# Performance work log

Hardware: AMD Instinct MI355X
Metric: run time of the kernel (lower is better)

The kernel has to match this reference:

```python
import jax, jax.numpy as jnp
import numpy as np

D_MODEL = 1024
NUM_HEADS = 16
D_K = D_MODEL // NUM_HEADS
ROPE_THETA = 10000.0
SEQ = 4096


def setup_inputs() -> dict:
    key = jax.random.key(0)
    ks = jax.random.split(key, 5)
    s = 1.0 / np.sqrt(D_MODEL)
    return {
        "x": jax.random.normal(ks[0], (1, SEQ, D_MODEL), jnp.float32),
        "token_positions": jnp.arange(SEQ, dtype=jnp.int32),
        "Wq": jax.random.normal(ks[1], (D_MODEL, D_MODEL), jnp.float32) * s,
        "Wk": jax.random.normal(ks[2], (D_MODEL, D_MODEL), jnp.float32) * s,
        "Wv": jax.random.normal(ks[3], (D_MODEL, D_MODEL), jnp.float32) * s,
        "Wo": jax.random.normal(ks[4], (D_MODEL, D_MODEL), jnp.float32) * s,
    }


def _rope(t, positions):
    # t: [b, h, s, d_k]; interleaved pair rotation
    half = D_K // 2
    inv_freq = ROPE_THETA ** (-jnp.arange(half, dtype=jnp.float32) * 2.0 / D_K)
    ang = positions.astype(jnp.float32)[:, None] * inv_freq[None, :]  # [s, half]
    cos, sin = jnp.cos(ang), jnp.sin(ang)
    x1 = t[..., 0::2]
    x2 = t[..., 1::2]
    r1 = x1 * cos - x2 * sin
    r2 = x1 * sin + x2 * cos
    return jnp.stack([r1, r2], axis=-1).reshape(t.shape)


def reference(x, token_positions, Wq, Wk, Wv, Wo):
    b, s, _ = x.shape
    def split_heads(t):
        return t.reshape(b, s, NUM_HEADS, D_K).transpose(0, 2, 1, 3)  # [b,h,s,dk]
    q = split_heads(x @ Wq.T)
    k = split_heads(x @ Wk.T)
    v = split_heads(x @ Wv.T)
    q = _rope(q, token_positions)
    k = _rope(k, token_positions)
    scores = jnp.einsum('bhqd,bhkd->bhqk', q, k) / np.sqrt(D_K)
    causal = jnp.tril(jnp.ones((s, s), dtype=bool))
    scores = jnp.where(causal, scores, -jnp.inf)
    attn = jax.nn.softmax(scores, axis=-1)
    out = jnp.einsum('bhqk,bhkd->bhqd', attn, v)
    out = out.transpose(0, 2, 1, 3).reshape(b, s, D_MODEL)
    return out @ Wo.T
```

## Files before the change

kernel.cpp:

```cpp
#include <hip/hip_runtime.h>

#define S    4096
#define DM   1024
#define H    16
#define DK   64

typedef __bf16 bf16;
typedef __bf16 bf16x8 __attribute__((ext_vector_type(8)));
typedef __bf16 bf16x4 __attribute__((ext_vector_type(4)));
typedef float  f32x4  __attribute__((ext_vector_type(4)));

__global__ __launch_bounds__(256)
void convert_kernel(const float* __restrict__ x,  const float* __restrict__ wq,
                    const float* __restrict__ wk, const float* __restrict__ wv,
                    const float* __restrict__ wo,
                    bf16* __restrict__ xb,  bf16* __restrict__ wqb,
                    bf16* __restrict__ wkb, bf16* __restrict__ wvb,
                    bf16* __restrict__ wob)
{
    const size_t i = (size_t)blockIdx.x * 256 + threadIdx.x;
    const float* src; bf16* dst; size_t off;
    if (i < 1048576)      { src = x;  dst = xb;  off = i; }
    else if (i < 1310720) { src = wq; dst = wqb; off = i - 1048576; }
    else if (i < 1572864) { src = wk; dst = wkb; off = i - 1310720; }
    else if (i < 1835008) { src = wv; dst = wvb; off = i - 1572864; }
    else                  { src = wo; dst = wob; off = i - 1835008; }
    f32x4 v = ((const f32x4*)src)[off];
    bf16x4 b;
    for (int r = 0; r < 4; r++) b[r] = (bf16)v[r];
    ((bf16x4*)dst)[off] = b;
}

__global__ __launch_bounds__(256)
void gemm_kernel(const bf16* __restrict__ A,
                 const bf16* __restrict__ w0, const bf16* __restrict__ w1,
                 const bf16* __restrict__ w2,
                 const int* __restrict__ pos,
                 bf16* __restrict__ o0, bf16* __restrict__ o1,
                 bf16* __restrict__ o2,
                 float* __restrict__ of,
                 int base_mode)
{
    const int z    = blockIdx.z;
    const int mode = base_mode + z;
    const bf16* W  = (z == 0) ? w0 : (z == 1 ? w1 : w2);
    bf16* Out      = (z == 0) ? o0 : (z == 1 ? o1 : o2);

    __shared__ bf16 As[64 * 72];
    __shared__ bf16 Bs[64 * 72];

    const int tid  = threadIdx.x;
    const int lane = tid & 63;
    const int wv   = tid >> 6;
    const int quad = lane >> 4;
    const int col  = lane & 15;
    const int wm   = wv >> 1, wn = wv & 1;

    const int tileM = blockIdx.x * 64;
    const int tileN = blockIdx.y * 64;

    const int ldRow = tid >> 2;
    const int ldK   = (tid & 3) * 16;

    f32x4 acc[2][2] = {};

    for (int kc = 0; kc < DM; kc += 64) {
        bf16x8 a0 = *(const bf16x8*)&A[(size_t)(tileM + ldRow) * DM + kc + ldK];
        bf16x8 a1 = *(const bf16x8*)&A[(size_t)(tileM + ldRow) * DM + kc + ldK + 8];
        bf16x8 b0 = *(const bf16x8*)&W[(size_t)(tileN + ldRow) * DM + kc + ldK];
        bf16x8 b1 = *(const bf16x8*)&W[(size_t)(tileN + ldRow) * DM + kc + ldK + 8];
        __syncthreads();
        *(bf16x8*)&As[ldRow * 72 + ldK]     = a0;
        *(bf16x8*)&As[ldRow * 72 + ldK + 8] = a1;
        *(bf16x8*)&Bs[ldRow * 72 + ldK]     = b0;
        *(bf16x8*)&Bs[ldRow * 72 + ldK + 8] = b1;
        __syncthreads();

        for (int kk = 0; kk < 2; kk++) {
            bf16x8 af0 = *(const bf16x8*)&As[(wm * 32 + 0 * 16 + col) * 72 + kk * 32 + quad * 8];
            bf16x8 af1 = *(const bf16x8*)&As[(wm * 32 + 1 * 16 + col) * 72 + kk * 32 + quad * 8];
            bf16x8 bf0 = *(const bf16x8*)&Bs[(wn * 32 + 0 * 16 + col) * 72 + kk * 32 + quad * 8];
            bf16x8 bf1 = *(const bf16x8*)&Bs[(wn * 32 + 1 * 16 + col) * 72 + kk * 32 + quad * 8];

            acc[0][0] = __builtin_amdgcn_mfma_f32_16x16x32_bf16(af0, bf0, acc[0][0], 0, 0, 0);
            acc[0][1] = __builtin_amdgcn_mfma_f32_16x16x32_bf16(af0, bf1, acc[0][1], 0, 0, 0);
            acc[1][0] = __builtin_amdgcn_mfma_f32_16x16x32_bf16(af1, bf0, acc[1][0], 0, 0, 0);
            acc[1][1] = __builtin_amdgcn_mfma_f32_16x16x32_bf16(af1, bf1, acc[1][1], 0, 0, 0);
        }
    }

    for (int fm = 0; fm < 2; fm++)
    for (int fn = 0; fn < 2; fn++) {
        f32x4 v = acc[fm][fn];
        const int n = tileN + wn * 32 + fn * 16 + col;
        for (int r = 0; r < 4; r++) {
            const int m = tileM + wm * 32 + fm * 16 + quad * 4 + r;
            float val = v[r];
            if (mode <= 1) {
                float part = __shfl_xor(val, 1);
                const int d = n & 63;
                const int i = d >> 1;
                float inv = exp2f(-(float)i * 0.41524101186092034f);
                float ang = (float)pos[m] * inv;
                float c = cosf(ang), sn = sinf(ang);
                float rot = (n & 1) ? (val * c + part * sn)
                                    : (val * c - part * sn);
                if (mode == 0) rot *= 0.18033688011112042f;
                Out[((size_t)(n >> 6) * S + m) * 64 + d] = (bf16)rot;
            } else if (mode == 2) {
                Out[(size_t)n * S + m] = (bf16)val;
            } else {
                of[(size_t)m * DM + n] = val;
            }
        }
    }
}

__global__ __launch_bounds__(256, 2)
void attn_kernel(const bf16* __restrict__ q, const bf16* __restrict__ k,
                 const bf16* __restrict__ vt,
                 bf16* __restrict__ P0g, bf16* __restrict__ P1g,
                 float* __restrict__ l0g, float* __restrict__ l1g)
{
    const int bid = blockIdx.x;
    const int xcd = bid & 7;
    const int b3  = (bid >> 3) & 1;
    const int u   = (bid >> 4) & 15;
    const int b8  = (bid >> 8) & 1;
    const int h   = (xcd << 1) | b8;
    const int z   = b3;
    const int QB  = (b3 == b8) ? (15 - u) : u;

    const int tid  = threadIdx.x;
    const int lane = tid & 63;
    const int wv   = tid >> 6;
    const int quad = lane >> 4;
    const int col  = lane & 15;

    const int T2  = 2 * QB + 2;
    const int kt0 = z * T2;
    const int kt1 = kt0 + T2;

    __shared__ bf16 Ks[64 * 72];
    __shared__ bf16 Vs[64 * 72];
    __shared__ bf16 plds[4][64 * 40];

    const int qbase = QB * 256 + wv * 64;

    bf16x8 qf[4][2];
#pragma unroll
    for (int qt = 0; qt < 4; qt++) {
        const bf16* qr = &q[((size_t)(h * S + qbase + qt * 16 + col)) * 64];
        qf[qt][0] = *(const bf16x8*)(qr + quad * 8);
        qf[qt][1] = *(const bf16x8*)(qr + 32 + quad * 8);
    }

    float li[4] = {};
    f32x4 o[4][4] = {};

    const int srow = tid >> 2;
    const int sseg = (tid & 3) * 16;
    const bf16* kg_ = k  + ((size_t)h * S) * 64;
    const bf16* vg_ = vt + ((size_t)h * 64) * S;

    bf16x8 kr0 = *(const bf16x8*)(kg_ + (size_t)(kt0 * 64 + srow) * 64 + sseg);
    bf16x8 kr1 = *(const bf16x8*)(kg_ + (size_t)(kt0 * 64 + srow) * 64 + sseg + 8);
    bf16x8 vr0 = *(const bf16x8*)(vg_ + (size_t)srow * S + kt0 * 64 + sseg);
    bf16x8 vr1 = *(const bf16x8*)(vg_ + (size_t)srow * S + kt0 * 64 + sseg + 8);

    for (int kt = kt0; kt < kt1; kt++) {
        const int kbase = kt * 64;

        __syncthreads();
        *(bf16x8*)&Ks[srow * 72 + sseg]     = kr0;
        *(bf16x8*)&Ks[srow * 72 + sseg + 8] = kr1;
        *(bf16x8*)&Vs[srow * 72 + sseg]     = vr0;
        *(bf16x8*)&Vs[srow * 72 + sseg + 8] = vr1;
        __syncthreads();

        if (kt + 1 < kt1) {
            const int nb = kbase + 64;
            kr0 = *(const bf16x8*)(kg_ + (size_t)(nb + srow) * 64 + sseg);
            kr1 = *(const bf16x8*)(kg_ + (size_t)(nb + srow) * 64 + sseg + 8);
            vr0 = *(const bf16x8*)(vg_ + (size_t)srow * S + nb + sseg);
            vr1 = *(const bf16x8*)(vg_ + (size_t)srow * S + nb + sseg + 8);
        }

        const bool diag = (kt >= (QB << 2));

#pragma unroll
        for (int half = 0; half < 2; half++) {
            __builtin_amdgcn_wave_barrier();
#pragma unroll
            for (int kg2 = 0; kg2 < 2; kg2++) {
                const int kg = half * 2 + kg2;
                bf16x8 kf0 = *(const bf16x8*)&Ks[(kg * 16 + col) * 72 + quad * 8];
                bf16x8 kf1 = *(const bf16x8*)&Ks[(kg * 16 + col) * 72 + 32 + quad * 8];

                f32x4 st[4];
                __builtin_amdgcn_s_setprio(1);
#pragma unroll
                for (int qt = 0; qt < 4; qt++) {
                    f32x4 zz = {};
                    zz = __builtin_amdgcn_mfma_f32_16x16x32_bf16(kf0, qf[qt][0], zz, 0, 0, 0);
                    zz = __builtin_amdgcn_mfma_f32_16x16x32_bf16(kf1, qf[qt][1], zz, 0, 0, 0);
                    st[qt] = zz;
                }
                __builtin_amdgcn_s_setprio(0);

                if (diag) {
#pragma unroll
                    for (int qt = 0; qt < 4; qt++) {
                        const int gq = qbase + qt * 16 + col;
#pragma unroll
                        for (int r = 0; r < 4; r++) {
                            const int gk = kbase + kg * 16 + quad * 4 + r;
                            st[qt][r] = (gk > gq) ? -1e30f : st[qt][r];
                        }
                    }
                }

#pragma unroll
                for (int qt = 0; qt < 4; qt++) {
                    bf16x4 pk;
#pragma unroll
                    for (int r = 0; r < 4; r++) {
                        float p;
                        asm("v_exp_f32 %0, %1" : "=v"(p) : "v"(st[qt][r]));
                        li[qt] += p;
                        pk[r] = (bf16)p;
                    }
                    *(bf16x4*)&plds[wv][(qt * 16 + col) * 40 + kg2 * 16 + quad * 4] = pk;
                }
            }

            __builtin_amdgcn_wave_barrier();

            bf16x8 pb[4];
#pragma unroll
            for (int qt = 0; qt < 4; qt++)
                pb[qt] = *(const bf16x8*)&plds[wv][(qt * 16 + col) * 40 + quad * 8];

            __builtin_amdgcn_s_setprio(1);
#pragma unroll
            for (int dg = 0; dg < 4; dg++) {
                bf16x8 va = *(const bf16x8*)&Vs[(dg * 16 + col) * 72 + half * 32 + quad * 8];
#pragma unroll
                for (int qt = 0; qt < 4; qt++)
                    o[dg][qt] = __builtin_amdgcn_mfma_f32_16x16x32_bf16(va, pb[qt], o[dg][qt], 0, 0, 0);
            }
            __builtin_amdgcn_s_setprio(0);
        }
    }

#pragma unroll
    for (int qt = 0; qt < 4; qt++) {
        li[qt] += __shfl_xor(li[qt], 16);
        li[qt] += __shfl_xor(li[qt], 32);
    }

    bf16*  Pz = z ? P1g : P0g;
    float* lz = z ? l1g : l0g;
#pragma unroll
    for (int dg = 0; dg < 4; dg++)
#pragma unroll
    for (int qt = 0; qt < 4; qt++) {
        const int gq = qbase + qt * 16 + col;
        bf16x4 ov;
#pragma unroll
        for (int r = 0; r < 4; r++) ov[r] = (bf16)o[dg][qt][r];
        *(bf16x4*)&Pz[(size_t)gq * DM + h * 64 + dg * 16 + quad * 4] = ov;
    }
    if (quad == 0) {
#pragma unroll
        for (int qt = 0; qt < 4; qt++)
            lz[(size_t)h * S + qbase + qt * 16 + col] = li[qt];
    }
}

__global__ __launch_bounds__(256)
void combine_kernel(const bf16* __restrict__ P0, const bf16* __restrict__ P1,
                    const float* __restrict__ l0, const float* __restrict__ l1,
                    bf16* __restrict__ ao)
{
    const size_t i    = (size_t)blockIdx.x * 256 + threadIdx.x;
    const size_t base = i * 8;
    const int s  = (int)(base >> 10);
    const int dm = (int)(base & 1023);
    const int h  = dm >> 6;
    const float rli = 1.f / (l0[(size_t)h * S + s] + l1[(size_t)h * S + s]);
    bf16x8 a = *(const bf16x8*)&P0[base];
    bf16x8 b = *(const bf16x8*)&P1[base];
    bf16x8 ov;
    for (int r = 0; r < 8; r++)
        ov[r] = (bf16)(((float)a[r] + (float)b[r]) * rli);
    *(bf16x8*)&ao[base] = ov;
}

extern "C" void kernel_launch(void* const* d_in, const int* in_sizes, int n_in,
                              void* d_out, int out_size, void* d_ws, size_t ws_size,
                              hipStream_t stream)
{
    const float* x   = (const float*)d_in[0];
    const int*   pos = (const int*)d_in[1];
    const float* Wq  = (const float*)d_in[2];
    const float* Wk  = (const float*)d_in[3];
    const float* Wv  = (const float*)d_in[4];
    const float* Wo  = (const float*)d_in[5];
    float* out = (float*)d_out;

    char* w = (char*)d_ws;
    bf16*  xb  = (bf16*)(w);
    bf16*  wqb = (bf16*)(w + (size_t) 8 * 1024 * 1024);
    bf16*  wkb = (bf16*)(w + (size_t)10 * 1024 * 1024);
    bf16*  wvb = (bf16*)(w + (size_t)12 * 1024 * 1024);
    bf16*  P0  = (bf16*)(w);
    bf16*  P1  = (bf16*)(w + (size_t) 8 * 1024 * 1024);
    bf16*  qb  = (bf16*)(w + (size_t)16 * 1024 * 1024);
    bf16*  kb  = (bf16*)(w + (size_t)24 * 1024 * 1024);
    bf16*  vt  = (bf16*)(w + (size_t)32 * 1024 * 1024);
    float* l0  = (float*)(w + (size_t)40 * 1024 * 1024);
    float* l1  = (float*)(w + (size_t)40 * 1024 * 1024 + 256 * 1024);
    bf16*  ao  = (bf16*)(w + (size_t)16 * 1024 * 1024);
    bf16*  wob = (bf16*)(w + (size_t)46 * 1024 * 1024);

    dim3 blk(256);
    convert_kernel<<<dim3(8192), blk, 0, stream>>>(x, Wq, Wk, Wv, Wo,
                                                   xb, wqb, wkb, wvb, wob);
    gemm_kernel<<<dim3(64, 16, 3), blk, 0, stream>>>(xb, wqb, wkb, wvb, pos,
                                                     qb, kb, vt, out, 0);
    attn_kernel<<<dim3(512), blk, 0, stream>>>(qb, kb, vt,
                                               P0, P1, l0, l1);
    combine_kernel<<<dim3(2048), blk, 0, stream>>>(P0, P1, l0, l1, ao);
    gemm_kernel<<<dim3(64, 16, 1), blk, 0, stream>>>(ao, wob, wob, wob, pos,
                                                     P0, P0, P0, out, 3);
}
```

Before: 230.0 us.

## Enlarge GEMM tiles to 128x128 and load tiles directly to LDS

The projection GEMM tile grows from 64x64 to 128x128, so each wave computes a 4x4 grid of MFMA fragments instead of 2x2. Operand tiles are now fetched with global_load_lds straight into LDS in a fragment-ordered layout, which removes the register staging and the padded row layout. The aim is more data reuse per LDS load and fewer global loads per FLOP. In exchange the grid has fewer blocks (768 for QKV, 256 for the output projection) and each thread holds more accumulator registers.

```diff
diff --git a/kernel.cpp b/kernel.cpp
--- a/kernel.cpp
+++ b/kernel.cpp
@@ -46,8 +46,8 @@
     const bf16* W  = (z == 0) ? w0 : (z == 1 ? w1 : w2);
     bf16* Out      = (z == 0) ? o0 : (z == 1 ? o1 : o2);
 
-    __shared__ bf16 As[64 * 72];
-    __shared__ bf16 Bs[64 * 72];
+    __shared__ bf16 As[16 * 512];
+    __shared__ bf16 Bs[16 * 512];
 
     const int tid  = threadIdx.x;
     const int lane = tid & 63;
@@ -56,45 +56,50 @@
     const int col  = lane & 15;
     const int wm   = wv >> 1, wn = wv & 1;
 
-    const int tileM = blockIdx.x * 64;
-    const int tileN = blockIdx.y * 64;
-
-    const int ldRow = tid >> 2;
-    const int ldK   = (tid & 3) * 16;
-
-    f32x4 acc[2][2] = {};
+    const int tileM = blockIdx.x * 128;
+    const int tileN = blockIdx.y * 128;
+
+    f32x4 acc[4][4] = {};
 
     for (int kc = 0; kc < DM; kc += 64) {
-        bf16x8 a0 = *(const bf16x8*)&A[(size_t)(tileM + ldRow) * DM + kc + ldK];
-        bf16x8 a1 = *(const bf16x8*)&A[(size_t)(tileM + ldRow) * DM + kc + ldK + 8];
-        bf16x8 b0 = *(const bf16x8*)&W[(size_t)(tileN + ldRow) * DM + kc + ldK];
-        bf16x8 b1 = *(const bf16x8*)&W[(size_t)(tileN + ldRow) * DM + kc + ldK + 8];
         __syncthreads();
-        *(bf16x8*)&As[ldRow * 72 + ldK]     = a0;
-        *(bf16x8*)&As[ldRow * 72 + ldK + 8] = a1;
-        *(bf16x8*)&Bs[ldRow * 72 + ldK]     = b0;
-        *(bf16x8*)&Bs[ldRow * 72 + ldK + 8] = b1;
+#pragma unroll
+        for (int i = 0; i < 4; i++) {
+            const int f  = wv * 4 + i;
+            const int rg = f >> 1, kk = f & 1;
+            const size_t go = (size_t)(rg * 16 + col) * DM + kc + kk * 32 + quad * 8;
+            __builtin_amdgcn_global_load_lds(
+                (const __attribute__((address_space(1))) void*)(A + (size_t)tileM * DM + go),
+                (__attribute__((address_space(3))) void*)&As[f * 512], 16, 0, 0);
+            __builtin_amdgcn_global_load_lds(
+                (const __attribute__((address_space(1))) void*)(W + (size_t)tileN * DM + go),
+                (__attribute__((address_space(3))) void*)&Bs[f * 512], 16, 0, 0);
+        }
         __syncthreads();
 
+#pragma unroll
         for (int kk = 0; kk < 2; kk++) {
-            bf16x8 af0 = *(const bf16x8*)&As[(wm * 32 + 0 * 16 + col) * 72 + kk * 32 + quad * 8];
-            bf16x8 af1 = *(const bf16x8*)&As[(wm * 32 + 1 * 16 + col) * 72 + kk * 32 + quad * 8];
-            bf16x8 bf0 = *(const bf16x8*)&Bs[(wn * 32 + 0 * 16 + col) * 72 + kk * 32 + quad * 8];
-            bf16x8 bf1 = *(const bf16x8*)&Bs[(wn * 32 + 1 * 16 + col) * 72 + kk * 32 + quad * 8];
-
-            acc[0][0] = __builtin_amdgcn_mfma_f32_16x16x32_bf16(af0, bf0, acc[0][0], 0, 0, 0);
-            acc[0][1] = __builtin_amdgcn_mfma_f32_16x16x32_bf16(af0, bf1, acc[0][1], 0, 0, 0);
-            acc[1][0] = __builtin_amdgcn_mfma_f32_16x16x32_bf16(af1, bf0, acc[1][0], 0, 0, 0);
-            acc[1][1] = __builtin_amdgcn_mfma_f32_16x16x32_bf16(af1, bf1, acc[1][1], 0, 0, 0);
-        }
-    }
-
-    for (int fm = 0; fm < 2; fm++)
-    for (int fn = 0; fn < 2; fn++) {
+            bf16x8 af[4], bfr[4];
+#pragma unroll
+            for (int fm = 0; fm < 4; fm++)
+                af[fm] = *(const bf16x8*)&As[(((wm * 4 + fm) << 1) | kk) * 512 + lane * 8];
+#pragma unroll
+            for (int fn = 0; fn < 4; fn++)
+                bfr[fn] = *(const bf16x8*)&Bs[(((wn * 4 + fn) << 1) | kk) * 512 + lane * 8];
+#pragma unroll
+            for (int fm = 0; fm < 4; fm++)
+#pragma unroll
+                for (int fn = 0; fn < 4; fn++)
+                    acc[fm][fn] = __builtin_amdgcn_mfma_f32_16x16x32_bf16(af[fm], bfr[fn], acc[fm][fn], 0, 0, 0);
+        }
+    }
+
+    for (int fm = 0; fm < 4; fm++)
+    for (int fn = 0; fn < 4; fn++) {
         f32x4 v = acc[fm][fn];
-        const int n = tileN + wn * 32 + fn * 16 + col;
+        const int n = tileN + wn * 64 + fn * 16 + col;
         for (int r = 0; r < 4; r++) {
-            const int m = tileM + wm * 32 + fm * 16 + quad * 4 + r;
+            const int m = tileM + wm * 64 + fm * 16 + quad * 4 + r;
             float val = v[r];
             if (mode <= 1) {
                 float part = __shfl_xor(val, 1);
@@ -327,11 +332,11 @@
     dim3 blk(256);
     convert_kernel<<<dim3(8192), blk, 0, stream>>>(x, Wq, Wk, Wv, Wo,
                                                    xb, wqb, wkb, wvb, wob);
-    gemm_kernel<<<dim3(64, 16, 3), blk, 0, stream>>>(xb, wqb, wkb, wvb, pos,
-                                                     qb, kb, vt, out, 0);
+    gemm_kernel<<<dim3(32, 8, 3), blk, 0, stream>>>(xb, wqb, wkb, wvb, pos,
+                                                    qb, kb, vt, out, 0);
     attn_kernel<<<dim3(512), blk, 0, stream>>>(qb, kb, vt,
                                                P0, P1, l0, l1);
     combine_kernel<<<dim3(2048), blk, 0, stream>>>(P0, P1, l0, l1, ao);
-    gemm_kernel<<<dim3(64, 16, 1), blk, 0, stream>>>(ao, wob, wob, wob, pos,
-                                                     P0, P0, P0, out, 3);
-}
+    gemm_kernel<<<dim3(32, 8, 1), blk, 0, stream>>>(ao, wob, wob, wob, pos,
+                                                    P0, P0, P0, out, 3);
+}
```

Result: slower. 588.6 us (+155.9%).

## Use 128x128 tiles with direct global-to-LDS loads for QKV projection

Applied to the files above, without the earlier changes.

The QKV projection GEMM moves to a dedicated kernel with 128x128 output tiles per block and a 4x4 MFMA fragment grid per wave, which raises data reuse per loaded byte. Operand tiles are loaded straight into LDS with global_load_lds in a fragment-major layout. The epilogue (RoPE, scaling, transposed V) is staged through shared memory so the stores to global memory are coalesced 16-byte writes. The output projection keeps the old 64x64 kernel, now specialised. The change risks higher register pressure and lower occupancy, has only 768 blocks, and loads each tile with no double buffering.

```diff
diff --git a/kernel.cpp b/kernel.cpp
--- a/kernel.cpp
+++ b/kernel.cpp
@@ -32,22 +32,21 @@
 }
 
 __global__ __launch_bounds__(256)
-void gemm_kernel(const bf16* __restrict__ A,
-                 const bf16* __restrict__ w0, const bf16* __restrict__ w1,
-                 const bf16* __restrict__ w2,
-                 const int* __restrict__ pos,
-                 bf16* __restrict__ o0, bf16* __restrict__ o1,
-                 bf16* __restrict__ o2,
-                 float* __restrict__ of,
-                 int base_mode)
-{
-    const int z    = blockIdx.z;
-    const int mode = base_mode + z;
-    const bf16* W  = (z == 0) ? w0 : (z == 1 ? w1 : w2);
-    bf16* Out      = (z == 0) ? o0 : (z == 1 ? o1 : o2);
-
-    __shared__ bf16 As[64 * 72];
-    __shared__ bf16 Bs[64 * 72];
+void gemm128_kernel(const bf16* __restrict__ A,
+                    const bf16* __restrict__ w0, const bf16* __restrict__ w1,
+                    const bf16* __restrict__ w2,
+                    const int* __restrict__ pos,
+                    bf16* __restrict__ o0, bf16* __restrict__ o1,
+                    bf16* __restrict__ o2)
+{
+    const int mode = blockIdx.z;
+    const bf16* W  = (mode == 0) ? w0 : (mode == 1 ? w1 : w2);
+    bf16* Out      = (mode == 0) ? o0 : (mode == 1 ? o1 : o2);
+
+    __shared__ bf16 smem[17408];
+    bf16* As = smem;
+    bf16* Bs = smem + 8192;
+    bf16* Cs = smem;
 
     const int tid  = threadIdx.x;
     const int lane = tid & 63;
@@ -56,6 +55,114 @@
     const int col  = lane & 15;
     const int wm   = wv >> 1, wn = wv & 1;
 
+    const int tileM = blockIdx.x * 128;
+    const int tileN = blockIdx.y * 128;
+
+    f32x4 acc[4][4] = {};
+
+    for (int kc = 0; kc < DM; kc += 64) {
+        __syncthreads();
+#pragma unroll
+        for (int i = 0; i < 4; i++) {
+            const int f  = wv * 4 + i;
+            const int rg = f >> 1, kk = f & 1;
+            const size_t go = (size_t)(rg * 16 + col) * DM + kc + kk * 32 + quad * 8;
+            __builtin_amdgcn_global_load_lds(
+                (const __attribute__((address_space(1))) void*)(A + (size_t)tileM * DM + go),
+                (__attribute__((address_space(3))) void*)&As[f * 512], 16, 0, 0);
+            __builtin_amdgcn_global_load_lds(
+                (const __attribute__((address_space(1))) void*)(W + (size_t)tileN * DM + go),
+                (__attribute__((address_space(3))) void*)&Bs[f * 512], 16, 0, 0);
+        }
+        __syncthreads();
+
+#pragma unroll
+        for (int kk = 0; kk < 2; kk++) {
+            bf16x8 af[4], bfr[4];
+#pragma unroll
+            for (int fm = 0; fm < 4; fm++)
+                af[fm] = *(const bf16x8*)&As[(((wm * 4 + fm) << 1) | kk) * 512 + lane * 8];
+#pragma unroll
+            for (int fn = 0; fn < 4; fn++)
+                bfr[fn] = *(const bf16x8*)&Bs[(((wn * 4 + fn) << 1) | kk) * 512 + lane * 8];
+#pragma unroll
+            for (int fm = 0; fm < 4; fm++)
+#pragma unroll
+                for (int fn = 0; fn < 4; fn++)
+                    acc[fm][fn] = __builtin_amdgcn_mfma_f32_16x16x32_bf16(af[fm], bfr[fn], acc[fm][fn], 0, 0, 0);
+        }
+    }
+
+    __syncthreads();
+
+    if (mode <= 1) {
+#pragma unroll
+        for (int fm = 0; fm < 4; fm++)
+#pragma unroll
+        for (int fn = 0; fn < 4; fn++) {
+            f32x4 v = acc[fm][fn];
+            const int nl = wn * 64 + fn * 16 + col;
+            const int d  = nl & 63;
+            const int ii = d >> 1;
+            const float inv = exp2f(-(float)ii * 0.41524101186092034f);
+#pragma unroll
+            for (int r = 0; r < 4; r++) {
+                const int m  = wm * 64 + fm * 16 + quad * 4 + r;
+                float val  = v[r];
+                float part = __shfl_xor(val, 1);
+                float ang  = (float)pos[tileM + m] * inv;
+                float c = cosf(ang), sn = sinf(ang);
+                float rot = (nl & 1) ? (val * c + part * sn)
+                                     : (val * c - part * sn);
+                if (mode == 0) rot *= 0.18033688011112042f;
+                Cs[m * 136 + nl] = (bf16)rot;
+            }
+        }
+    } else {
+#pragma unroll
+        for (int fm = 0; fm < 4; fm++)
+#pragma unroll
+        for (int fn = 0; fn < 4; fn++) {
+            const int nl    = wn * 64 + fn * 16 + col;
+            const int mbase = wm * 64 + fm * 16 + quad * 4;
+            bf16x4 pk;
+#pragma unroll
+            for (int r = 0; r < 4; r++) pk[r] = (bf16)acc[fm][fn][r];
+            *(bf16x4*)&Cs[nl * 136 + mbase] = pk;
+        }
+    }
+    __syncthreads();
+
+#pragma unroll
+    for (int i = 0; i < 8; i++) {
+        const int c   = i * 256 + tid;
+        const int row = c >> 4;
+        const int off = (c & 15) * 8;
+        bf16x8 vv = *(const bf16x8*)&Cs[row * 136 + off];
+        if (mode <= 1) {
+            const int head = blockIdx.y * 2 + (off >> 6);
+            *(bf16x8*)&Out[((size_t)head * S + tileM + row) * 64 + (off & 63)] = vv;
+        } else {
+            *(bf16x8*)&Out[(size_t)(tileN + row) * S + tileM + off] = vv;
+        }
+    }
+}
+
+__global__ __launch_bounds__(256)
+void gemm64_kernel(const bf16* __restrict__ A,
+                   const bf16* __restrict__ W,
+                   float* __restrict__ of)
+{
+    __shared__ bf16 As[64 * 72];
+    __shared__ bf16 Bs[64 * 72];
+
+    const int tid  = threadIdx.x;
+    const int lane = tid & 63;
+    const int wv   = tid >> 6;
+    const int quad = lane >> 4;
+    const int col  = lane & 15;
+    const int wm   = wv >> 1, wn = wv & 1;
+
     const int tileM = blockIdx.x * 64;
     const int tileN = blockIdx.y * 64;
 
@@ -95,23 +202,7 @@
         const int n = tileN + wn * 32 + fn * 16 + col;
         for (int r = 0; r < 4; r++) {
             const int m = tileM + wm * 32 + fm * 16 + quad * 4 + r;
-            float val = v[r];
-            if (mode <= 1) {
-                float part = __shfl_xor(val, 1);
-                const int d = n & 63;
-                const int i = d >> 1;
-                float inv = exp2f(-(float)i * 0.41524101186092034f);
-                float ang = (float)pos[m] * inv;
-                float c = cosf(ang), sn = sinf(ang);
-                float rot = (n & 1) ? (val * c + part * sn)
-                                    : (val * c - part * sn);
-                if (mode == 0) rot *= 0.18033688011112042f;
-                Out[((size_t)(n >> 6) * S + m) * 64 + d] = (bf16)rot;
-            } else if (mode == 2) {
-                Out[(size_t)n * S + m] = (bf16)val;
-            } else {
-                of[(size_t)m * DM + n] = val;
-            }
+            of[(size_t)m * DM + n] = v[r];
         }
     }
 }
@@ -327,11 +418,10 @@
     dim3 blk(256);
     convert_kernel<<<dim3(8192), blk, 0, stream>>>(x, Wq, Wk, Wv, Wo,
                                                    xb, wqb, wkb, wvb, wob);
-    gemm_kernel<<<dim3(64, 16, 3), blk, 0, stream>>>(xb, wqb, wkb, wvb, pos,
-                                                     qb, kb, vt, out, 0);
+    gemm128_kernel<<<dim3(32, 8, 3), blk, 0, stream>>>(xb, wqb, wkb, wvb, pos,
+                                                       qb, kb, vt);
     attn_kernel<<<dim3(512), blk, 0, stream>>>(qb, kb, vt,
                                                P0, P1, l0, l1);
     combine_kernel<<<dim3(2048), blk, 0, stream>>>(P0, P1, l0, l1, ao);
-    gemm_kernel<<<dim3(64, 16, 1), blk, 0, stream>>>(ao, wob, wob, wob, pos,
-                                                     P0, P0, P0, out, 3);
-}
+    gemm64_kernel<<<dim3(64, 16), blk, 0, stream>>>(ao, wob, out);
+}
```

After: 476.6 us. 2.07x slower.
